# Performance work log

Measured on AMD Instinct MI355X. Metric: run time of the kernel, lower is better.

The kernel has to match this reference:

```python
import jax, jax.numpy as jnp
from jax import lax
import numpy as np

B, P, N = 4, 12000, 100   # batch, max_pillars, max_points_per_pillar
H, W = 108, 124           # pseudo-image size from forward()
DN = ('NCHW', 'HWIO', 'NCHW')


def _conv(x, k, b):
    y = lax.conv_general_dilated(x, k, (1, 1), 'SAME', dimension_numbers=DN)
    return y + b[None, :, None, None]


def _cbr(x, k, b, s, t):
    # Conv2d + folded BatchNorm2d (eval: per-channel scale/shift) + ReLU
    y = _conv(x, k, b)
    return jax.nn.relu(y * s[None, :, None, None] + t[None, :, None, None])


def _pool(x):
    return lax.reduce_window(x, -jnp.inf, lax.max, (1, 1, 2, 2), (1, 1, 2, 2), 'VALID')


def setup_inputs() -> dict:
    key = jax.random.key(0)
    ks = iter(jax.random.split(key, 64))
    d = {}
    d['pillars'] = jax.random.normal(next(ks), (B, P, N, 9), jnp.float32)

    def w(shape, scale=0.05):
        return jax.random.normal(next(ks), shape, jnp.float32) * scale

    d['w1'] = w((9, 64)); d['b1'] = w((64,))
    d['s1'] = 1.0 + w((64,)); d['t1'] = w((64,))
    d['w2'] = w((64, 64)); d['b2'] = w((64,))
    d['s2'] = 1.0 + w((64,)); d['t2'] = w((64,))
    chans = [(64, 64), (64, 64), (64, 128), (128, 128), (128, 256), (256, 256)]
    for i, (ci, co) in enumerate(chans, 1):
        d['ck%d' % i] = w((3, 3, ci, co)); d['cb%d' % i] = w((co,))
        d['cs%d' % i] = 1.0 + w((co,)); d['ct%d' % i] = w((co,))
    d['hk1'] = w((3, 3, 256, 256)); d['hb1'] = w((256,))
    d['hk2'] = w((1, 1, 256, 10)); d['hb2'] = w((10,))
    d['num_points'] = jax.random.randint(next(ks), (B, P), 0, 100, jnp.int32)
    return d


def reference(pillars, w1, b1, s1, t1, w2, b2, s2, t2,
              ck1, cb1, cs1, ct1, ck2, cb2, cs2, ct2,
              ck3, cb3, cs3, ct3, ck4, cb4, cs4, ct4,
              ck5, cb5, cs5, ct5, ck6, cb6, cs6, ct6,
              hk1, hb1, hk2, hb2, num_points):
    # pillar feature net: Linear+BN(folded)+ReLU x2, batched over all points  [B,P,N,9] -> [B,P,N,64]
    h = jax.nn.relu((pillars @ w1 + b1) * s1 + t1)
    h = jax.nn.relu((h @ w2 + b2) * s2 + t2)
    # masked segment-max over the variable-length point groups
    mask = jnp.arange(N)[None, None, :] < num_points[:, :, None]          # [B,P,N]
    neg = jnp.finfo(h.dtype).min
    feat = jnp.max(jnp.where(mask[..., None], h, neg), axis=2)            # [B,P,64]
    valid = num_points > 0
    feat = jnp.where(valid[..., None], feat, 0.0)
    cnt = jnp.maximum(jnp.sum(valid, axis=1), 1).astype(feat.dtype)       # [B]
    mean = jnp.sum(feat, axis=1) / cnt[:, None]                           # [B,64]
    # nearest-interpolate a 1x1 map to HxW == broadcast
    x = jnp.broadcast_to(mean[:, :, None, None], (pillars.shape[0], 64, H, W))
    # 2D backbone
    x = _cbr(x, ck1, cb1, cs1, ct1); x = _cbr(x, ck2, cb2, cs2, ct2); x = _pool(x)
    x = _cbr(x, ck3, cb3, cs3, ct3); x = _cbr(x, ck4, cb4, cs4, ct4); x = _pool(x)
    x = _cbr(x, ck5, cb5, cs5, ct5); x = _cbr(x, ck6, cb6, cs6, ct6)
    # detection head
    y = jax.nn.relu(_conv(x, hk1, hb1))
    return _conv(y, hk2, hb2)   # [B, num_classes+7=10, 27, 31]
```

## Files before the change

kernel.cpp:

```cpp
#include <hip/hip_runtime.h>

typedef __bf16 vbf8 __attribute__((ext_vector_type(8)));
typedef __bf16 vbf4 __attribute__((ext_vector_type(4)));
typedef unsigned short us8 __attribute__((ext_vector_type(8)));
typedef float f32x4 __attribute__((ext_vector_type(4)));
typedef float f32x4u __attribute__((ext_vector_type(4), aligned(4)));

__global__ void setup_kernel(const float* __restrict__ w1, const float* __restrict__ b1,
                             const float* __restrict__ s1, const float* __restrict__ t1,
                             const float* __restrict__ w2, const float* __restrict__ b2,
                             const float* __restrict__ s2, const float* __restrict__ t2,
                             __bf16* __restrict__ wfrag, float* __restrict__ be2f) {
  int l = threadIdx.x;
  int s = l & 15, g = l >> 4;
#pragma unroll
  for (int m = 0; m < 4; ++m) {
    int c = 32 * (m & 1) + 8 * (s >> 2) + 4 * (m >> 1) + (s & 3);
#pragma unroll
    for (int e = 0; e < 8; ++e) {
      int k = g * 8 + e;
      float v = 0.f;
      if (k < 9)       v = w1[k * 64 + c] * s1[c];
      else if (k == 9) v = fmaf(b1[c], s1[c], t1[c]);
      wfrag[(m * 64 + l) * 8 + e] = (__bf16)v;
    }
    int co = s + 16 * m;
#pragma unroll
    for (int e = 0; e < 8; ++e) {
      int k = g * 8 + e;
      wfrag[((4 + m) * 64 + l) * 8 + e] = (__bf16)(w2[k * 64 + co] * s2[co]);
      wfrag[((8 + m) * 64 + l) * 8 + e] = (__bf16)(w2[(32 + k) * 64 + co] * s2[co]);
    }
    be2f[m * 64 + l] = fmaf(b2[co], s2[co], t2[co]);
  }
}

__global__ __launch_bounds__(256) void convw_kernel(
    const float* __restrict__ k1, const float* __restrict__ k2,
    const float* __restrict__ k3, const float* __restrict__ k4,
    const float* __restrict__ k5, const float* __restrict__ k6,
    const float* __restrict__ kh, __bf16* __restrict__ wT) {
  __shared__ float tile[64][65];
  const int tCI[7]    = {64, 64, 64, 128, 128, 256, 256};
  const int tCO[7]    = {64, 64, 128, 128, 256, 256, 256};
  const int tOFF[7]   = {0, 36864, 73728, 147456, 294912, 589824, 1179648};
  const int tTILES[7] = {9, 9, 18, 36, 72, 144, 144};
  int bid = blockIdx.x;
  int ti = 0, acc = 0;
  while (ti < 6 && bid >= acc + tTILES[ti]) { acc += tTILES[ti]; ++ti; }
  int lt = bid - acc;
  int CI = tCI[ti], CO = tCO[ti];
  const float* src;
  if (ti == 0) src = k1; else if (ti == 1) src = k2; else if (ti == 2) src = k3;
  else if (ti == 3) src = k4; else if (ti == 4) src = k5; else if (ti == 5) src = k6;
  else src = kh;
  int cot = CO / 64, tpt = (CI / 64) * cot;
  int tap = lt / tpt; int r2 = lt - tap * tpt;
  int ci0 = (r2 / cot) * 64, co0 = (r2 % cot) * 64;
  const float* sp = src + (size_t)(tap * CI + ci0) * CO + co0;
  int t = threadIdx.x;
  int lr = t >> 6, lc = t & 63;
#pragma unroll
  for (int rr = 0; rr < 64; rr += 4)
    tile[rr + lr][lc] = sp[(size_t)(rr + lr) * CO + lc];
  __syncthreads();
  __bf16* dst = wT + tOFF[ti] + ((size_t)tap * CO + co0) * CI + ci0;
#pragma unroll
  for (int rr = 0; rr < 64; rr += 4)
    dst[(size_t)(rr + lr) * CI + lc] = (__bf16)tile[lc][rr + lr];
}

__global__ void zero_borders_kernel(__bf16* __restrict__ a64, __bf16* __restrict__ b64,
                                    __bf16* __restrict__ c128a, __bf16* __restrict__ c128b,
                                    __bf16* __restrict__ c256a, __bf16* __restrict__ c256b) {
  int idx = blockIdx.x * 256 + threadIdx.x;
  __bf16* buf; int H2, C, p;
  if (idx < 34848)       { buf = (idx < 17424) ? a64 : b64;     H2 = 66; C = 64;  p = idx % 17424; }
  else if (idx < 44096)  { int q = idx - 34848; buf = (q < 4624) ? c128a : c128b; H2 = 34; C = 128; p = q % 4624; }
  else if (idx < 46688)  { int q = idx - 44096; buf = (q < 1296) ? c256a : c256b; H2 = 18; C = 256; p = q % 1296; }
  else return;
  int w = p % H2; int h = (p / H2) % H2;
  if (h != 0 && h != H2 - 1 && w != 0 && w != H2 - 1) return;
  us8 zz = {0, 0, 0, 0, 0, 0, 0, 0};
  __bf16* q = buf + (size_t)p * C;
  for (int c = 0; c < C; c += 8) *(us8*)(q + c) = zz;
}

__global__ __launch_bounds__(256) void pillar_kernel(
    const float* __restrict__ pil, const int* __restrict__ npt,
    const __bf16* __restrict__ wfrag, const float* __restrict__ be2f,
    float* __restrict__ partial, int* __restrict__ pcnt)
{
  __shared__ float redf[4][64];
  __shared__ int redc[4];
  const int tid = threadIdx.x;
  const int wv = tid >> 6, lane = tid & 63;
  const int s = lane & 15, g = lane >> 4;
  const int wid = blockIdx.x * 4 + wv;
  const int b = wid / 6000;
  const int p0 = (wid - b * 6000) * 2;

  vbf8 w1f[4], w2f0[4], w2f1[4];
  float be2[4];
#pragma unroll
  for (int m = 0; m < 4; ++m) {
    w1f[m]  = *(const vbf8*)(wfrag + ((0 + m) * 64 + lane) * 8);
    w2f0[m] = *(const vbf8*)(wfrag + ((4 + m) * 64 + lane) * 8);
    w2f1[m] = *(const vbf8*)(wfrag + ((8 + m) * 64 + lane) * 8);
    be2[m] = be2f[m * 64 + lane];
  }

  float fsum[4] = {0.f, 0.f, 0.f, 0.f};
  int cnt = 0;

  for (int i = 0; i < 2; ++i) {
    int pidx = b * 12000 + p0 + i;
    int np = npt[pidx];
    if (np <= 0) continue;
    ++cnt;
    float feat[4][4];
#pragma unroll
    for (int n = 0; n < 4; ++n)
#pragma unroll
      for (int r = 0; r < 4; ++r) feat[n][r] = 0.f;

    int ngrp = (np + 15) >> 4;
    const float* pbase = pil + (size_t)pidx * 900;
    for (int grp = 0; grp < ngrp; ++grp) {
      int pt = grp * 16 + s; pt = min(pt, 99);
      const float* ptp = pbase + pt * 9;
      f32x4u lo = *(const f32x4u*)ptp;
      f32x4u hi = *(const f32x4u*)(ptp + 4);
      float v8 = ptp[8];
      vbf8 b1f;
      b1f[0] = (__bf16)(g == 0 ? lo[0] : (g == 1 ? v8 : 0.f));
      b1f[1] = (__bf16)(g == 0 ? lo[1] : (g == 1 ? 1.0f : 0.f));
      b1f[2] = (__bf16)(g == 0 ? lo[2] : 0.f);
      b1f[3] = (__bf16)(g == 0 ? lo[3] : 0.f);
      b1f[4] = (__bf16)(g == 0 ? hi[0] : 0.f);
      b1f[5] = (__bf16)(g == 0 ? hi[1] : 0.f);
      b1f[6] = (__bf16)(g == 0 ? hi[2] : 0.f);
      b1f[7] = (__bf16)(g == 0 ? hi[3] : 0.f);

      const f32x4 z = {0.f, 0.f, 0.f, 0.f};
      f32x4 d1[4];
#pragma unroll
      for (int m = 0; m < 4; ++m)
        d1[m] = __builtin_amdgcn_mfma_f32_16x16x32_bf16(w1f[m], b1f, z, 0, 0, 0);

      vbf8 a2f0, a2f1;
#pragma unroll
      for (int r = 0; r < 4; ++r) {
        a2f0[r]     = (__bf16)fmaxf(d1[0][r], 0.f);
        a2f1[r]     = (__bf16)fmaxf(d1[1][r], 0.f);
        a2f0[4 + r] = (__bf16)fmaxf(d1[2][r], 0.f);
        a2f1[4 + r] = (__bf16)fmaxf(d1[3][r], 0.f);
      }

      f32x4 d2[4];
#pragma unroll
      for (int n = 0; n < 4; ++n) {
        f32x4 cb = {be2[n], be2[n], be2[n], be2[n]};
        d2[n] = __builtin_amdgcn_mfma_f32_16x16x32_bf16(a2f0, w2f0[n], cb, 0, 0, 0);
        d2[n] = __builtin_amdgcn_mfma_f32_16x16x32_bf16(a2f1, w2f1[n], d2[n], 0, 0, 0);
      }
      if (((grp + 1) << 4) <= np) {
#pragma unroll
        for (int n = 0; n < 4; ++n)
#pragma unroll
          for (int r = 0; r < 4; ++r) feat[n][r] = fmaxf(feat[n][r], d2[n][r]);
      } else {
#pragma unroll
        for (int n = 0; n < 4; ++n)
#pragma unroll
          for (int r = 0; r < 4; ++r) {
            float vv = (grp * 16 + 4 * g + r < np) ? d2[n][r] : 0.f;
            feat[n][r] = fmaxf(feat[n][r], vv);
          }
      }
    }
#pragma unroll
    for (int n = 0; n < 4; ++n) {
      float m = fmaxf(fmaxf(feat[n][0], feat[n][1]), fmaxf(feat[n][2], feat[n][3]));
      m = fmaxf(m, __shfl_xor(m, 16));
      m = fmaxf(m, __shfl_xor(m, 32));
      fsum[n] += m;
    }
  }
  if (g == 0) {
#pragma unroll
    for (int n = 0; n < 4; ++n) redf[wv][s + 16 * n] = fsum[n];
  }
  if (lane == 0) redc[wv] = cnt;
  __syncthreads();
  if (tid < 64) {
    float tot = redf[0][tid] + redf[1][tid] + redf[2][tid] + redf[3][tid];
    partial[blockIdx.x * 64 + tid] = tot;
    if (tid == 0) pcnt[blockIdx.x] = redc[0] + redc[1] + redc[2] + redc[3];
  }
}

__global__ void mean_kernel(const float* __restrict__ partial,
                            const int* __restrict__ pcnt,
                            float* __restrict__ mean) {
  int b = blockIdx.x, t = threadIdx.x;
  int c = t & 63, q = t >> 6;
  float sum = 0.f;
  for (int w = q; w < 1500; w += 4) sum += partial[(b * 1500 + w) * 64 + c];
  int cl = 0;
  for (int w = t; w < 1500; w += 256) cl += pcnt[b * 1500 + w];
  __shared__ float sh[256];
  __shared__ int shc[256];
  sh[t] = sum; shc[t] = cl;
  __syncthreads();
  for (int o = 128; o > 0; o >>= 1) {
    if (t < o) shc[t] += shc[t + o];
    __syncthreads();
  }
  if (t < 64) {
    float tot = sh[t] + sh[t + 64] + sh[t + 128] + sh[t + 192];
    mean[b * 64 + t] = tot / (float)(shc[0] > 0 ? shc[0] : 1);
  }
}

__global__ void broadcast_kernel(const float* __restrict__ mean,
                                 __bf16* __restrict__ x0) {
  int idx = blockIdx.x * 256 + threadIdx.x;
  int c8 = idx & 7; int rest = idx >> 3;
  int w = rest & 63; rest >>= 6;
  int h = rest & 63; int b = rest >> 6;
  const float* mb = mean + b * 64 + c8 * 8;
  vbf8 v;
#pragma unroll
  for (int e = 0; e < 8; ++e) v[e] = (__bf16)mb[e];
  *(vbf8*)(x0 + (((size_t)(b * 66 + h + 1) * 66) + (w + 1)) * 64 + c8 * 8) = v;
}

template <int CIN, int COUT, int HW>
__global__ __launch_bounds__(256) void kconv_kernel(
    const __bf16* __restrict__ x, const __bf16* __restrict__ wt,
    float* __restrict__ kpart)
{
  constexpr int H2 = HW + 2;
  constexpr int NT = COUT / 64;
  constexpr int KC = CIN / 32;
  constexpr int MTOT = 4 * HW * HW;
  constexpr int LOG = (HW == 64) ? 6 : (HW == 32) ? 5 : 4;
  const int tid = threadIdx.x, wv = tid >> 6, lane = tid & 63;
  const int s = lane & 15, g = lane >> 4;
  const int task = blockIdx.x * 4 + wv;
  const int kg = task % 3;
  const int t2 = task / 3;
  const int nt = t2 % NT;
  const int mt = t2 / NT;
  const int m0 = mt * 32;
  const int b = m0 >> (2 * LOG);
  const int mb = m0 - (b << (2 * LOG));

  size_t arow[2];
#pragma unroll
  for (int mf = 0; mf < 2; ++mf) {
    int m = mb + mf * 16 + s;
    int hh = m >> LOG, ww = m & (HW - 1);
    arow[mf] = ((size_t)(b * H2 + hh) * H2 + ww) * CIN;
  }

  f32x4 acc[2][4];
#pragma unroll
  for (int mf = 0; mf < 2; ++mf)
#pragma unroll
    for (int nf = 0; nf < 4; ++nf) acc[mf][nf] = (f32x4){0.f, 0.f, 0.f, 0.f};

#pragma unroll
  for (int j = 0; j < 3; ++j) {
    const int tap = kg * 3 + j;
    const int dh = tap / 3, dw = tap % 3;
    const size_t aoff = ((size_t)dh * H2 + dw) * CIN + 8 * g;
    const __bf16* wtap = wt + ((size_t)tap * COUT + nt * 64) * CIN + 8 * g;
#pragma unroll 2
    for (int ck = 0; ck < KC; ++ck) {
      vbf8 a0 = *(const vbf8*)(x + arow[0] + aoff + ck * 32);
      vbf8 a1 = *(const vbf8*)(x + arow[1] + aoff + ck * 32);
#pragma unroll
      for (int nf = 0; nf < 4; ++nf) {
        vbf8 bb = *(const vbf8*)(wtap + (size_t)(nf * 16 + s) * CIN + ck * 32);
        acc[0][nf] = __builtin_amdgcn_mfma_f32_16x16x32_bf16(a0, bb, acc[0][nf], 0, 0, 0);
        acc[1][nf] = __builtin_amdgcn_mfma_f32_16x16x32_bf16(a1, bb, acc[1][nf], 0, 0, 0);
      }
    }
  }

  float* kp = kpart + (size_t)kg * MTOT * COUT;
#pragma unroll
  for (int mf = 0; mf < 2; ++mf)
#pragma unroll
    for (int nf = 0; nf < 4; ++nf) {
      int co = nt * 64 + nf * 16 + s;
#pragma unroll
      for (int r = 0; r < 4; ++r) {
        int m = m0 + mf * 16 + 4 * g + r;
        kp[(size_t)m * COUT + co] = acc[mf][nf][r];
      }
    }
}

template <int COUT, int HW, bool HAS_BN, bool OUT_F32>
__global__ __launch_bounds__(256) void reduce_kernel(
    const float* __restrict__ kpart, const float* __restrict__ cb,
    const float* __restrict__ cs, const float* __restrict__ ct,
    __bf16* __restrict__ ypad, float* __restrict__ yf32)
{
  constexpr int H2 = HW + 2;
  constexpr int MTOT = 4 * HW * HW;
  constexpr int CQ = COUT / 4;
  constexpr int LOG = (HW == 64) ? 6 : (HW == 32) ? 5 : 4;
  int idx = blockIdx.x * 256 + threadIdx.x;
  int cq = idx % CQ; int m = idx / CQ;
  int co0 = cq * 4;
  const f32x4* f4 = (const f32x4*)kpart;
  f32x4 v = f4[(size_t)m * CQ + cq];
  f32x4 v1 = f4[((size_t)MTOT + m) * CQ + cq];
  f32x4 v2 = f4[((size_t)2 * MTOT + m) * CQ + cq];
  v += v1 + v2;
  f32x4 r;
  if (HAS_BN) {
    f32x4 sc = *(const f32x4*)(cs + co0);
    f32x4 bb = *(const f32x4*)(cb + co0);
    f32x4 tt = *(const f32x4*)(ct + co0);
#pragma unroll
    for (int e = 0; e < 4; ++e) r[e] = fmaxf(fmaf(v[e], sc[e], fmaf(bb[e], sc[e], tt[e])), 0.f);
  } else {
    f32x4 bb = *(const f32x4*)(cb + co0);
#pragma unroll
    for (int e = 0; e < 4; ++e) r[e] = fmaxf(v[e] + bb[e], 0.f);
  }
  if constexpr (OUT_F32) {
    *(f32x4*)(yf32 + (size_t)m * COUT + co0) = r;
  } else {
    int b = m >> (2 * LOG);
    int mm = m - (b << (2 * LOG));
    int hh = mm >> LOG, ww = mm & (HW - 1);
    vbf4 o;
#pragma unroll
    for (int e = 0; e < 4; ++e) o[e] = (__bf16)r[e];
    *(vbf4*)(ypad + (((size_t)(b * H2 + hh + 1) * H2) + ww + 1) * COUT + co0) = o;
  }
}

template <int C, int HI>
__global__ void pool_kernel(const __bf16* __restrict__ x, __bf16* __restrict__ y) {
  constexpr int HO = HI / 2, W2I = HI + 2, W2O = HO + 2, C8 = C / 8;
  int idx = blockIdx.x * 256 + threadIdx.x;
  if (idx >= 4 * W2O * W2O * C8) return;
  int c8 = idx % C8; int rest = idx / C8;
  int wo = rest % W2O; rest /= W2O;
  int ho = rest % W2O; int b = rest / W2O;
  us8 out;
  if (ho == 0 || ho == W2O - 1 || wo == 0 || wo == W2O - 1) {
    out = (us8){0, 0, 0, 0, 0, 0, 0, 0};
  } else {
    int hi = 2 * (ho - 1) + 1, wi = 2 * (wo - 1) + 1;
    const unsigned short* p =
        (const unsigned short*)x + (((size_t)(b * W2I + hi) * W2I) + wi) * C + c8 * 8;
    us8 v0 = *(const us8*)p;
    us8 v1 = *(const us8*)(p + C);
    us8 v2 = *(const us8*)(p + (size_t)W2I * C);
    us8 v3 = *(const us8*)(p + (size_t)W2I * C + C);
#pragma unroll
    for (int e = 0; e < 8; ++e) {
      unsigned short a = v0[e] > v1[e] ? v0[e] : v1[e];
      unsigned short c = v2[e] > v3[e] ? v2[e] : v3[e];
      out[e] = a > c ? a : c;
    }
  }
  *(us8*)((unsigned short*)y + (((size_t)(b * W2O + ho) * W2O) + wo) * C + c8 * 8) = out;
}

__global__ void head2_kernel(const float* __restrict__ x, const float* __restrict__ wk,
                             const float* __restrict__ bias, float* __restrict__ y) {
  int h = blockIdx.x, b = blockIdx.y;
  int t = threadIdx.x;
  int co = t & 15, w = t >> 4;
  if (co >= 10) return;
  const float* xr = x + ((size_t)(b * 16 + h) * 16 + w) * 256;
  float acc = 0.f;
#pragma unroll 4
  for (int ci = 0; ci < 256; ci += 4) {
    float4 in4 = *(const float4*)(xr + ci);
    acc = fmaf(in4.x, wk[(ci + 0) * 10 + co], acc);
    acc = fmaf(in4.y, wk[(ci + 1) * 10 + co], acc);
    acc = fmaf(in4.z, wk[(ci + 2) * 10 + co], acc);
    acc = fmaf(in4.w, wk[(ci + 3) * 10 + co], acc);
  }
  y[((size_t)(b * 16 + h) * 16 + w) * 10 + co] = acc + bias[co];
}

__global__ void scatter_kernel(const float* __restrict__ y, float* __restrict__ out) {
  int idx = blockIdx.x * 256 + threadIdx.x;
  if (idx >= 4 * 10 * 27 * 31) return;
  int c = idx % 31;
  int r = (idx / 31) % 27;
  int ch = (idx / (31 * 27)) % 10;
  int b = idx / (31 * 27 * 10);
  int rr = (r <= 7) ? r : ((r >= 20) ? r - 11 : 7);
  int cc = (c <= 7) ? c : ((c >= 24) ? c - 15 : 7);
  out[idx] = y[((size_t)(b * 16 + rr) * 16 + cc) * 10 + ch];
}

extern "C" void kernel_launch(void* const* d_in, const int* in_sizes, int n_in,
                              void* d_out, int out_size, void* d_ws, size_t ws_size,
                              hipStream_t stream) {
  (void)in_sizes; (void)n_in; (void)out_size; (void)ws_size;
  const float* pillars = (const float*)d_in[0];
  const float* w1 = (const float*)d_in[1];
  const float* b1 = (const float*)d_in[2];
  const float* s1 = (const float*)d_in[3];
  const float* t1 = (const float*)d_in[4];
  const float* w2 = (const float*)d_in[5];
  const float* b2 = (const float*)d_in[6];
  const float* s2 = (const float*)d_in[7];
  const float* t2 = (const float*)d_in[8];
  const float* ck[6], *cbv[6], *csv[6], *ctv[6];
  for (int i = 0; i < 6; ++i) {
    ck[i]  = (const float*)d_in[9 + i * 4];
    cbv[i] = (const float*)d_in[10 + i * 4];
    csv[i] = (const float*)d_in[11 + i * 4];
    ctv[i] = (const float*)d_in[12 + i * 4];
  }
  const float* hk1 = (const float*)d_in[33];
  const float* hb1 = (const float*)d_in[34];
  const float* hk2 = (const float*)d_in[35];
  const float* hb2 = (const float*)d_in[36];
  const int* num_points = (const int*)d_in[37];
  float* out = (float*)d_out;

  char* wsb = (char*)d_ws;
  size_t off = 0;
  auto alloc = [&](size_t n) { char* p = wsb + off; off = (off + n + 255) & ~(size_t)255; return p; };
  float*  kpart  = (float*)alloc(12582912);
  float*  ppart  = (float*)alloc(1536000);
  int*    pcnt   = (int*)alloc(24000);
  float*  mean   = (float*)alloc(1024);
  __bf16* wfrag  = (__bf16*)alloc(12288);
  float*  be2f   = (float*)alloc(1024);
  float*  h2out  = (float*)alloc(40960);
  __bf16* wT     = (__bf16*)alloc(3538944);
  __bf16* A64    = (__bf16*)alloc(2230272);
  __bf16* B64    = (__bf16*)alloc(2230272);
  __bf16* PL64   = (__bf16*)alloc(591872);
  __bf16* C128A  = (__bf16*)alloc(1183744);
  __bf16* C128B  = (__bf16*)alloc(1183744);
  __bf16* PL128  = (__bf16*)alloc(331776);
  __bf16* C256A  = (__bf16*)alloc(663552);
  __bf16* C256B  = (__bf16*)alloc(663552);
  float*  h1out  = (float*)alloc(1048576);

  __bf16* wt1 = wT + 0;       __bf16* wt2 = wT + 36864;
  __bf16* wt3 = wT + 73728;   __bf16* wt4 = wT + 147456;
  __bf16* wt5 = wT + 294912;  __bf16* wt6 = wT + 589824;
  __bf16* wth = wT + 1179648;

  setup_kernel<<<1, 64, 0, stream>>>(w1, b1, s1, t1, w2, b2, s2, t2, wfrag, be2f);
  convw_kernel<<<432, 256, 0, stream>>>(ck[0], ck[1], ck[2], ck[3], ck[4], ck[5],
                                        hk1, wT);
  zero_borders_kernel<<<183, 256, 0, stream>>>(A64, B64, C128A, C128B, C256A, C256B);

  pillar_kernel<<<6000, 256, 0, stream>>>(pillars, num_points, wfrag, be2f,
                                          ppart, pcnt);
  mean_kernel<<<4, 256, 0, stream>>>(ppart, pcnt, mean);
  broadcast_kernel<<<512, 256, 0, stream>>>(mean, A64);

  kconv_kernel<64, 64, 64><<<384, 256, 0, stream>>>(A64, wt1, kpart);
  reduce_kernel<64, 64, true, false><<<1024, 256, 0, stream>>>(
      kpart, cbv[0], csv[0], ctv[0], B64, nullptr);
  kconv_kernel<64, 64, 64><<<384, 256, 0, stream>>>(B64, wt2, kpart);
  reduce_kernel<64, 64, true, false><<<1024, 256, 0, stream>>>(
      kpart, cbv[1], csv[1], ctv[1], A64, nullptr);
  pool_kernel<64, 64><<<145, 256, 0, stream>>>(A64, PL64);
  kconv_kernel<64, 128, 32><<<192, 256, 0, stream>>>(PL64, wt3, kpart);
  reduce_kernel<128, 32, true, false><<<512, 256, 0, stream>>>(
      kpart, cbv[2], csv[2], ctv[2], C128A, nullptr);
  kconv_kernel<128, 128, 32><<<192, 256, 0, stream>>>(C128A, wt4, kpart);
  reduce_kernel<128, 32, true, false><<<512, 256, 0, stream>>>(
      kpart, cbv[3], csv[3], ctv[3], C128B, nullptr);
  pool_kernel<128, 32><<<81, 256, 0, stream>>>(C128B, PL128);
  kconv_kernel<128, 256, 16><<<96, 256, 0, stream>>>(PL128, wt5, kpart);
  reduce_kernel<256, 16, true, false><<<256, 256, 0, stream>>>(
      kpart, cbv[4], csv[4], ctv[4], C256A, nullptr);
  kconv_kernel<256, 256, 16><<<96, 256, 0, stream>>>(C256A, wt6, kpart);
  reduce_kernel<256, 16, true, false><<<256, 256, 0, stream>>>(
      kpart, cbv[5], csv[5], ctv[5], C256B, nullptr);
  kconv_kernel<256, 256, 16><<<96, 256, 0, stream>>>(C256B, wth, kpart);
  reduce_kernel<256, 16, false, true><<<256, 256, 0, stream>>>(
      kpart, hb1, nullptr, nullptr, nullptr, h1out);

  head2_kernel<<<dim3(16, 4), 256, 0, stream>>>(h1out, hk2, hb2, h2out);
  scatter_kernel<<<131, 256, 0, stream>>>(h2out, out);
}
```

Baseline: 340.8 us.

## Compute backbone only on distinct border-case positions of constant input

Because the backbone input is a spatially constant broadcast, every layer's output depends only on distance to the image border. The dense convolutions are replaced by 'case' convolutions that compute one representative per row/column border class (2E+1 classes) and map taps through caseof/repof indexing. Conv, bias, BN and ReLU are fused into one kernel, which drops the split-K partial buffer, the reduce kernels, the border zeroing and the broadcast kernel. This relies on the broadcast structure that the reference itself defines, so it holds for any input values. The cost is far fewer tiny launches with little parallelism each.

```diff
diff --git a/kernel.cpp b/kernel.cpp
--- a/kernel.cpp
+++ b/kernel.cpp
@@ -5,6 +5,16 @@
 typedef unsigned short us8 __attribute__((ext_vector_type(8)));
 typedef float f32x4 __attribute__((ext_vector_type(4)));
 typedef float f32x4u __attribute__((ext_vector_type(4), aligned(4)));
+
+__device__ __forceinline__ int caseof(int h, int H, int e) {
+  if (h < 0 || h >= H) return -1;
+  if (h < e) return h;
+  if (h >= H - e) return h - (H - 1) + 2 * e;
+  return e;
+}
+__device__ __forceinline__ int repof(int i, int H, int eo) {
+  return (i <= eo) ? i : H - 1 - 2 * eo + i;
+}
 
 __global__ void setup_kernel(const float* __restrict__ w1, const float* __restrict__ b1,
                              const float* __restrict__ s1, const float* __restrict__ t1,
@@ -70,22 +80,6 @@
     dst[(size_t)(rr + lr) * CI + lc] = (__bf16)tile[lc][rr + lr];
 }
 
-__global__ void zero_borders_kernel(__bf16* __restrict__ a64, __bf16* __restrict__ b64,
-                                    __bf16* __restrict__ c128a, __bf16* __restrict__ c128b,
-                                    __bf16* __restrict__ c256a, __bf16* __restrict__ c256b) {
-  int idx = blockIdx.x * 256 + threadIdx.x;
-  __bf16* buf; int H2, C, p;
-  if (idx < 34848)       { buf = (idx < 17424) ? a64 : b64;     H2 = 66; C = 64;  p = idx % 17424; }
-  else if (idx < 44096)  { int q = idx - 34848; buf = (q < 4624) ? c128a : c128b; H2 = 34; C = 128; p = q % 4624; }
-  else if (idx < 46688)  { int q = idx - 44096; buf = (q < 1296) ? c256a : c256b; H2 = 18; C = 256; p = q % 1296; }
-  else return;
-  int w = p % H2; int h = (p / H2) % H2;
-  if (h != 0 && h != H2 - 1 && w != 0 && w != H2 - 1) return;
-  us8 zz = {0, 0, 0, 0, 0, 0, 0, 0};
-  __bf16* q = buf + (size_t)p * C;
-  for (int c = 0; c < C; c += 8) *(us8*)(q + c) = zz;
-}
-
 __global__ __launch_bounds__(256) void pillar_kernel(
     const float* __restrict__ pil, const int* __restrict__ npt,
     const __bf16* __restrict__ wfrag, const float* __restrict__ be2f,
@@ -202,8 +196,10 @@
 
 __global__ void mean_kernel(const float* __restrict__ partial,
                             const int* __restrict__ pcnt,
-                            float* __restrict__ mean) {
+                            float* __restrict__ mean, __bf16* __restrict__ x0,
+                            __bf16* __restrict__ zbuf) {
   int b = blockIdx.x, t = threadIdx.x;
+  if (b == 0) zbuf[t] = (__bf16)0.f;
   int c = t & 63, q = t >> 6;
   float sum = 0.f;
   for (int w = q; w < 1500; w += 4) sum += partial[(b * 1500 + w) * 64 + c];
@@ -219,50 +215,49 @@
   }
   if (t < 64) {
     float tot = sh[t] + sh[t + 64] + sh[t + 128] + sh[t + 192];
-    mean[b * 64 + t] = tot / (float)(shc[0] > 0 ? shc[0] : 1);
-  }
-}
-
-__global__ void broadcast_kernel(const float* __restrict__ mean,
-                                 __bf16* __restrict__ x0) {
-  int idx = blockIdx.x * 256 + threadIdx.x;
-  int c8 = idx & 7; int rest = idx >> 3;
-  int w = rest & 63; rest >>= 6;
-  int h = rest & 63; int b = rest >> 6;
-  const float* mb = mean + b * 64 + c8 * 8;
-  vbf8 v;
-#pragma unroll
-  for (int e = 0; e < 8; ++e) v[e] = (__bf16)mb[e];
-  *(vbf8*)(x0 + (((size_t)(b * 66 + h + 1) * 66) + (w + 1)) * 64 + c8 * 8) = v;
-}
-
-template <int CIN, int COUT, int HW>
-__global__ __launch_bounds__(256) void kconv_kernel(
-    const __bf16* __restrict__ x, const __bf16* __restrict__ wt,
-    float* __restrict__ kpart)
+    float mv = tot / (float)(shc[0] > 0 ? shc[0] : 1);
+    mean[b * 64 + t] = mv;
+    x0[b * 64 + t] = (__bf16)mv;
+  }
+}
+
+template <int CI, int CO, int H, int EIN, bool HAS_BN, bool OUT_F32>
+__global__ __launch_bounds__(256) void caseconv_kernel(
+    const __bf16* __restrict__ xin, const __bf16* __restrict__ wt,
+    const float* __restrict__ cb, const float* __restrict__ cs,
+    const float* __restrict__ ct, __bf16* __restrict__ yout,
+    float* __restrict__ yf32, const __bf16* __restrict__ zbuf)
 {
-  constexpr int H2 = HW + 2;
-  constexpr int NT = COUT / 64;
-  constexpr int KC = CIN / 32;
-  constexpr int MTOT = 4 * HW * HW;
-  constexpr int LOG = (HW == 64) ? 6 : (HW == 32) ? 5 : 4;
+  constexpr int EOUT = EIN + 1;
+  constexpr int NBI = 2 * EIN + 1;
+  constexpr int NBO = 2 * EOUT + 1;
+  constexpr int M = NBO * NBO * 4;
+  constexpr int NT = CO / 64;
+  constexpr int KC = CI / 32;
+  constexpr int MT = (M + 31) / 32;
   const int tid = threadIdx.x, wv = tid >> 6, lane = tid & 63;
   const int s = lane & 15, g = lane >> 4;
   const int task = blockIdx.x * 4 + wv;
-  const int kg = task % 3;
-  const int t2 = task / 3;
-  const int nt = t2 % NT;
-  const int mt = t2 / NT;
-  const int m0 = mt * 32;
-  const int b = m0 >> (2 * LOG);
-  const int mb = m0 - (b << (2 * LOG));
-
-  size_t arow[2];
+  if (task >= MT * NT) return;
+  const int nt = task % NT, mt = task / NT;
+
+  const __bf16* pa[2][9];
 #pragma unroll
   for (int mf = 0; mf < 2; ++mf) {
-    int m = mb + mf * 16 + s;
-    int hh = m >> LOG, ww = m & (HW - 1);
-    arow[mf] = ((size_t)(b * H2 + hh) * H2 + ww) * CIN;
+    int m = mt * 32 + mf * 16 + s; if (m >= M) m = M - 1;
+    int b = m & 3, q = m >> 2;
+    int bw = q % NBO, bh = q / NBO;
+    int reph = repof(bh, H, EOUT), repw = repof(bw, H, EOUT);
+#pragma unroll
+    for (int dh = 0; dh < 3; ++dh)
+#pragma unroll
+      for (int dw = 0; dw < 3; ++dw) {
+        int jh = caseof(reph + dh - 1, H, EIN);
+        int jw = caseof(repw + dw - 1, H, EIN);
+        bool v = (jh >= 0) && (jw >= 0);
+        pa[mf][dh * 3 + dw] =
+            v ? xin + (size_t)((jh * NBI + jw) * 4 + b) * CI : zbuf;
+      }
   }
 
   f32x4 acc[2][4];
@@ -272,117 +267,79 @@
     for (int nf = 0; nf < 4; ++nf) acc[mf][nf] = (f32x4){0.f, 0.f, 0.f, 0.f};
 
 #pragma unroll
-  for (int j = 0; j < 3; ++j) {
-    const int tap = kg * 3 + j;
-    const int dh = tap / 3, dw = tap % 3;
-    const size_t aoff = ((size_t)dh * H2 + dw) * CIN + 8 * g;
-    const __bf16* wtap = wt + ((size_t)tap * COUT + nt * 64) * CIN + 8 * g;
-#pragma unroll 2
+  for (int tap = 0; tap < 9; ++tap) {
+    const __bf16* wtap = wt + ((size_t)tap * CO + nt * 64) * CI + 8 * g;
+#pragma unroll
     for (int ck = 0; ck < KC; ++ck) {
-      vbf8 a0 = *(const vbf8*)(x + arow[0] + aoff + ck * 32);
-      vbf8 a1 = *(const vbf8*)(x + arow[1] + aoff + ck * 32);
+      vbf8 a0 = *(const vbf8*)(pa[0][tap] + ck * 32 + 8 * g);
+      vbf8 a1 = *(const vbf8*)(pa[1][tap] + ck * 32 + 8 * g);
 #pragma unroll
       for (int nf = 0; nf < 4; ++nf) {
-        vbf8 bb = *(const vbf8*)(wtap + (size_t)(nf * 16 + s) * CIN + ck * 32);
+        vbf8 bb = *(const vbf8*)(wtap + (size_t)(nf * 16 + s) * CI + ck * 32);
         acc[0][nf] = __builtin_amdgcn_mfma_f32_16x16x32_bf16(a0, bb, acc[0][nf], 0, 0, 0);
         acc[1][nf] = __builtin_amdgcn_mfma_f32_16x16x32_bf16(a1, bb, acc[1][nf], 0, 0, 0);
       }
     }
   }
 
-  float* kp = kpart + (size_t)kg * MTOT * COUT;
-#pragma unroll
-  for (int mf = 0; mf < 2; ++mf)
-#pragma unroll
-    for (int nf = 0; nf < 4; ++nf) {
-      int co = nt * 64 + nf * 16 + s;
+#pragma unroll
+  for (int nf = 0; nf < 4; ++nf) {
+    int co = nt * 64 + nf * 16 + s;
+    float sc, sh;
+    if (HAS_BN) { sc = cs[co]; sh = fmaf(cb[co], sc, ct[co]); }
+    else        { sc = 1.f;    sh = cb[co]; }
+#pragma unroll
+    for (int mf = 0; mf < 2; ++mf)
 #pragma unroll
       for (int r = 0; r < 4; ++r) {
-        int m = m0 + mf * 16 + 4 * g + r;
-        kp[(size_t)m * COUT + co] = acc[mf][nf][r];
-      }
-    }
-}
-
-template <int COUT, int HW, bool HAS_BN, bool OUT_F32>
-__global__ __launch_bounds__(256) void reduce_kernel(
-    const float* __restrict__ kpart, const float* __restrict__ cb,
-    const float* __restrict__ cs, const float* __restrict__ ct,
-    __bf16* __restrict__ ypad, float* __restrict__ yf32)
-{
-  constexpr int H2 = HW + 2;
-  constexpr int MTOT = 4 * HW * HW;
-  constexpr int CQ = COUT / 4;
-  constexpr int LOG = (HW == 64) ? 6 : (HW == 32) ? 5 : 4;
+        int m = mt * 32 + mf * 16 + 4 * g + r;
+        if (m < M) {
+          float v = fmaxf(fmaf(acc[mf][nf][r], sc, sh), 0.f);
+          if constexpr (OUT_F32) yf32[(size_t)m * CO + co] = v;
+          else                   yout[(size_t)m * CO + co] = (__bf16)v;
+        }
+      }
+  }
+}
+
+template <int C, int HOUT, int EIN>
+__global__ void casepool_kernel(const __bf16* __restrict__ xin,
+                                __bf16* __restrict__ yout) {
+  constexpr int EOUT = (EIN + 1) / 2;
+  constexpr int NBI = 2 * EIN + 1;
+  constexpr int NBO = 2 * EOUT + 1;
+  constexpr int C8 = C / 8;
   int idx = blockIdx.x * 256 + threadIdx.x;
-  int cq = idx % CQ; int m = idx / CQ;
-  int co0 = cq * 4;
-  const f32x4* f4 = (const f32x4*)kpart;
-  f32x4 v = f4[(size_t)m * CQ + cq];
-  f32x4 v1 = f4[((size_t)MTOT + m) * CQ + cq];
-  f32x4 v2 = f4[((size_t)2 * MTOT + m) * CQ + cq];
-  v += v1 + v2;
-  f32x4 r;
-  if (HAS_BN) {
-    f32x4 sc = *(const f32x4*)(cs + co0);
-    f32x4 bb = *(const f32x4*)(cb + co0);
-    f32x4 tt = *(const f32x4*)(ct + co0);
-#pragma unroll
-    for (int e = 0; e < 4; ++e) r[e] = fmaxf(fmaf(v[e], sc[e], fmaf(bb[e], sc[e], tt[e])), 0.f);
-  } else {
-    f32x4 bb = *(const f32x4*)(cb + co0);
-#pragma unroll
-    for (int e = 0; e < 4; ++e) r[e] = fmaxf(v[e] + bb[e], 0.f);
-  }
-  if constexpr (OUT_F32) {
-    *(f32x4*)(yf32 + (size_t)m * COUT + co0) = r;
-  } else {
-    int b = m >> (2 * LOG);
-    int mm = m - (b << (2 * LOG));
-    int hh = mm >> LOG, ww = mm & (HW - 1);
-    vbf4 o;
-#pragma unroll
-    for (int e = 0; e < 4; ++e) o[e] = (__bf16)r[e];
-    *(vbf4*)(ypad + (((size_t)(b * H2 + hh + 1) * H2) + ww + 1) * COUT + co0) = o;
-  }
-}
-
-template <int C, int HI>
-__global__ void pool_kernel(const __bf16* __restrict__ x, __bf16* __restrict__ y) {
-  constexpr int HO = HI / 2, W2I = HI + 2, W2O = HO + 2, C8 = C / 8;
+  if (idx >= NBO * NBO * 4 * C8) return;
+  int c8 = idx % C8; int rest = idx / C8;
+  int b = rest & 3; int pos = rest >> 2;
+  int iw = pos % NBO, ih = pos / NBO;
+  int rh = repof(ih, HOUT, EOUT), rw = repof(iw, HOUT, EOUT);
+  int h0 = caseof(2 * rh, 2 * HOUT, EIN), h1 = caseof(2 * rh + 1, 2 * HOUT, EIN);
+  int w0 = caseof(2 * rw, 2 * HOUT, EIN), w1 = caseof(2 * rw + 1, 2 * HOUT, EIN);
+  const unsigned short* xp = (const unsigned short*)xin;
+  us8 v00 = *(const us8*)(xp + (size_t)((h0 * NBI + w0) * 4 + b) * C + c8 * 8);
+  us8 v01 = *(const us8*)(xp + (size_t)((h0 * NBI + w1) * 4 + b) * C + c8 * 8);
+  us8 v10 = *(const us8*)(xp + (size_t)((h1 * NBI + w0) * 4 + b) * C + c8 * 8);
+  us8 v11 = *(const us8*)(xp + (size_t)((h1 * NBI + w1) * 4 + b) * C + c8 * 8);
+  us8 o;
+#pragma unroll
+  for (int e = 0; e < 8; ++e) {
+    unsigned short a = v00[e] > v01[e] ? v00[e] : v01[e];
+    unsigned short c = v10[e] > v11[e] ? v10[e] : v11[e];
+    o[e] = a > c ? a : c;
+  }
+  *(us8*)((unsigned short*)yout + (size_t)((ih * NBO + iw) * 4 + b) * C + c8 * 8) = o;
+}
+
+__global__ void head2c_kernel(const float* __restrict__ x, const float* __restrict__ wk,
+                              const float* __restrict__ bias, float* __restrict__ y) {
   int idx = blockIdx.x * 256 + threadIdx.x;
-  if (idx >= 4 * W2O * W2O * C8) return;
-  int c8 = idx % C8; int rest = idx / C8;
-  int wo = rest % W2O; rest /= W2O;
-  int ho = rest % W2O; int b = rest / W2O;
-  us8 out;
-  if (ho == 0 || ho == W2O - 1 || wo == 0 || wo == W2O - 1) {
-    out = (us8){0, 0, 0, 0, 0, 0, 0, 0};
-  } else {
-    int hi = 2 * (ho - 1) + 1, wi = 2 * (wo - 1) + 1;
-    const unsigned short* p =
-        (const unsigned short*)x + (((size_t)(b * W2I + hi) * W2I) + wi) * C + c8 * 8;
-    us8 v0 = *(const us8*)p;
-    us8 v1 = *(const us8*)(p + C);
-    us8 v2 = *(const us8*)(p + (size_t)W2I * C);
-    us8 v3 = *(const us8*)(p + (size_t)W2I * C + C);
-#pragma unroll
-    for (int e = 0; e < 8; ++e) {
-      unsigned short a = v0[e] > v1[e] ? v0[e] : v1[e];
-      unsigned short c = v2[e] > v3[e] ? v2[e] : v3[e];
-      out[e] = a > c ? a : c;
-    }
-  }
-  *(us8*)((unsigned short*)y + (((size_t)(b * W2O + ho) * W2O) + wo) * C + c8 * 8) = out;
-}
-
-__global__ void head2_kernel(const float* __restrict__ x, const float* __restrict__ wk,
-                             const float* __restrict__ bias, float* __restrict__ y) {
-  int h = blockIdx.x, b = blockIdx.y;
-  int t = threadIdx.x;
-  int co = t & 15, w = t >> 4;
+  if (idx >= 121 * 4 * 16) return;
+  int co = idx & 15;
   if (co >= 10) return;
-  const float* xr = x + ((size_t)(b * 16 + h) * 16 + w) * 256;
+  int q = idx >> 4;
+  const float* xr = x + (size_t)q * 256;
   float acc = 0.f;
 #pragma unroll 4
   for (int ci = 0; ci < 256; ci += 4) {
@@ -392,7 +349,7 @@
     acc = fmaf(in4.z, wk[(ci + 2) * 10 + co], acc);
     acc = fmaf(in4.w, wk[(ci + 3) * 10 + co], acc);
   }
-  y[((size_t)(b * 16 + h) * 16 + w) * 10 + co] = acc + bias[co];
+  y[(size_t)q * 10 + co] = acc + bias[co];
 }
 
 __global__ void scatter_kernel(const float* __restrict__ y, float* __restrict__ out) {
@@ -404,7 +361,8 @@
   int b = idx / (31 * 27 * 10);
   int rr = (r <= 7) ? r : ((r >= 20) ? r - 11 : 7);
   int cc = (c <= 7) ? c : ((c >= 24) ? c - 15 : 7);
-  out[idx] = y[((size_t)(b * 16 + rr) * 16 + cc) * 10 + ch];
+  int ph = caseof(rr, 16, 5), pw = caseof(cc, 16, 5);
+  out[idx] = y[(size_t)(((ph * 11 + pw) * 4 + b)) * 10 + ch];
 }
 
 extern "C" void kernel_launch(void* const* d_in, const int* in_sizes, int n_in,
@@ -437,23 +395,24 @@
   char* wsb = (char*)d_ws;
   size_t off = 0;
   auto alloc = [&](size_t n) { char* p = wsb + off; off = (off + n + 255) & ~(size_t)255; return p; };
-  float*  kpart  = (float*)alloc(12582912);
-  float*  ppart  = (float*)alloc(1536000);
-  int*    pcnt   = (int*)alloc(24000);
-  float*  mean   = (float*)alloc(1024);
-  __bf16* wfrag  = (__bf16*)alloc(12288);
-  float*  be2f   = (float*)alloc(1024);
-  float*  h2out  = (float*)alloc(40960);
-  __bf16* wT     = (__bf16*)alloc(3538944);
-  __bf16* A64    = (__bf16*)alloc(2230272);
-  __bf16* B64    = (__bf16*)alloc(2230272);
-  __bf16* PL64   = (__bf16*)alloc(591872);
-  __bf16* C128A  = (__bf16*)alloc(1183744);
-  __bf16* C128B  = (__bf16*)alloc(1183744);
-  __bf16* PL128  = (__bf16*)alloc(331776);
-  __bf16* C256A  = (__bf16*)alloc(663552);
-  __bf16* C256B  = (__bf16*)alloc(663552);
-  float*  h1out  = (float*)alloc(1048576);
+  float*  ppart = (float*)alloc(1536000);
+  int*    pcnt  = (int*)alloc(24000);
+  float*  mean  = (float*)alloc(1024);
+  __bf16* wfrag = (__bf16*)alloc(12288);
+  float*  be2f  = (float*)alloc(1024);
+  __bf16* wT    = (__bf16*)alloc(3538944);
+  __bf16* zbuf  = (__bf16*)alloc(512);
+  __bf16* X0    = (__bf16*)alloc(512);
+  __bf16* X1    = (__bf16*)alloc(4608);
+  __bf16* X2    = (__bf16*)alloc(12800);
+  __bf16* P1    = (__bf16*)alloc(4608);
+  __bf16* X3    = (__bf16*)alloc(25600);
+  __bf16* X4    = (__bf16*)alloc(50176);
+  __bf16* P2    = (__bf16*)alloc(25600);
+  __bf16* X5    = (__bf16*)alloc(100352);
+  __bf16* X6    = (__bf16*)alloc(165888);
+  float*  XH    = (float*)alloc(495616);
+  float*  h2out = (float*)alloc(19360);
 
   __bf16* wt1 = wT + 0;       __bf16* wt2 = wT + 36864;
   __bf16* wt3 = wT + 73728;   __bf16* wt4 = wT + 147456;
@@ -463,37 +422,27 @@
   setup_kernel<<<1, 64, 0, stream>>>(w1, b1, s1, t1, w2, b2, s2, t2, wfrag, be2f);
   convw_kernel<<<432, 256, 0, stream>>>(ck[0], ck[1], ck[2], ck[3], ck[4], ck[5],
                                         hk1, wT);
-  zero_borders_kernel<<<183, 256, 0, stream>>>(A64, B64, C128A, C128B, C256A, C256B);
-
   pillar_kernel<<<6000, 256, 0, stream>>>(pillars, num_points, wfrag, be2f,
                                           ppart, pcnt);
-  mean_kernel<<<4, 256, 0, stream>>>(ppart, pcnt, mean);
-  broadcast_kernel<<<512, 256, 0, stream>>>(mean, A64);
-
-  kconv_kernel<64, 64, 64><<<384, 256, 0, stream>>>(A64, wt1, kpart);
-  reduce_kernel<64, 64, true, false><<<1024, 256, 0, stream>>>(
-      kpart, cbv[0], csv[0], ctv[0], B64, nullptr);
-  kconv_kernel<64, 64, 64><<<384, 256, 0, stream>>>(B64, wt2, kpart);
-  reduce_kernel<64, 64, true, false><<<1024, 256, 0, stream>>>(
-      kpart, cbv[1], csv[1], ctv[1], A64, nullptr);
-  pool_kernel<64, 64><<<145, 256, 0, stream>>>(A64, PL64);
-  kconv_kernel<64, 128, 32><<<192, 256, 0, stream>>>(PL64, wt3, kpart);
-  reduce_kernel<128, 32, true, false><<<512, 256, 0, stream>>>(
-      kpart, cbv[2], csv[2], ctv[2], C128A, nullptr);
-  kconv_kernel<128, 128, 32><<<192, 256, 0, stream>>>(C128A, wt4, kpart);
-  reduce_kernel<128, 32, true, false><<<512, 256, 0, stream>>>(
-      kpart, cbv[3], csv[3], ctv[3], C128B, nullptr);
-  pool_kernel<128, 32><<<81, 256, 0, stream>>>(C128B, PL128);
-  kconv_kernel<128, 256, 16><<<96, 256, 0, stream>>>(PL128, wt5, kpart);
-  reduce_kernel<256, 16, true, false><<<256, 256, 0, stream>>>(
-      kpart, cbv[4], csv[4], ctv[4], C256A, nullptr);
-  kconv_kernel<256, 256, 16><<<96, 256, 0, stream>>>(C256A, wt6, kpart);
-  reduce_kernel<256, 16, true, false><<<256, 256, 0, stream>>>(
-      kpart, cbv[5], csv[5], ctv[5], C256B, nullptr);
-  kconv_kernel<256, 256, 16><<<96, 256, 0, stream>>>(C256B, wth, kpart);
-  reduce_kernel<256, 16, false, true><<<256, 256, 0, stream>>>(
-      kpart, hb1, nullptr, nullptr, nullptr, h1out);
-
-  head2_kernel<<<dim3(16, 4), 256, 0, stream>>>(h1out, hk2, hb2, h2out);
+  mean_kernel<<<4, 256, 0, stream>>>(ppart, pcnt, mean, X0, zbuf);
+
+  caseconv_kernel<64, 64, 64, 0, true, false><<<1, 256, 0, stream>>>(
+      X0, wt1, cbv[0], csv[0], ctv[0], X1, nullptr, zbuf);
+  caseconv_kernel<64, 64, 64, 1, true, false><<<1, 256, 0, stream>>>(
+      X1, wt2, cbv[1], csv[1], ctv[1], X2, nullptr, zbuf);
+  casepool_kernel<64, 32, 2><<<2, 256, 0, stream>>>(X2, P1);
+  caseconv_kernel<64, 128, 32, 1, true, false><<<2, 256, 0, stream>>>(
+      P1, wt3, cbv[2], csv[2], ctv[2], X3, nullptr, zbuf);
+  caseconv_kernel<128, 128, 32, 2, true, false><<<4, 256, 0, stream>>>(
+      X3, wt4, cbv[3], csv[3], ctv[3], X4, nullptr, zbuf);
+  casepool_kernel<128, 16, 3><<<7, 256, 0, stream>>>(X4, P2);
+  caseconv_kernel<128, 256, 16, 2, true, false><<<7, 256, 0, stream>>>(
+      P2, wt5, cbv[4], csv[4], ctv[4], X5, nullptr, zbuf);
+  caseconv_kernel<256, 256, 16, 3, true, false><<<11, 256, 0, stream>>>(
+      X5, wt6, cbv[5], csv[5], ctv[5], X6, nullptr, zbuf);
+  caseconv_kernel<256, 256, 16, 4, false, true><<<16, 256, 0, stream>>>(
+      X6, wth, hb1, nullptr, nullptr, nullptr, XH, zbuf);
+
+  head2c_kernel<<<31, 256, 0, stream>>>(XH, hk2, hb2, h2out);
   scatter_kernel<<<131, 256, 0, stream>>>(h2out, out);
 }
```

New measurement: 438.0 us. +28.5%, slower.
